# Performance work log

Hardware: AMD Instinct MI355X
Metric: run time of the kernel (lower is better)

Reference implementation:

```python
import jax, jax.numpy as jnp
import numpy as np

B, S, D, H = 4, 2048, 1024, 16
DH = D // H  # 64


def setup_inputs() -> dict:
    key = jax.random.key(0)
    ks = jax.random.split(key, 9)
    scale = 1.0 / np.sqrt(D)
    x = jax.random.normal(ks[0], (B, S, D), dtype=jnp.float32)
    # Stacked per-head projection weights, equivalent to ModuleList of Linear(D, DH)
    Wq = jax.random.uniform(ks[1], (H, D, DH), jnp.float32, -scale, scale)
    bq = jax.random.uniform(ks[2], (H, DH), jnp.float32, -scale, scale)
    Wk = jax.random.uniform(ks[3], (H, D, DH), jnp.float32, -scale, scale)
    bk = jax.random.uniform(ks[4], (H, DH), jnp.float32, -scale, scale)
    Wv = jax.random.uniform(ks[5], (H, D, DH), jnp.float32, -scale, scale)
    bv = jax.random.uniform(ks[6], (H, DH), jnp.float32, -scale, scale)
    Wo = jax.random.uniform(ks[7], (D, D), jnp.float32, -scale, scale)
    bo = jax.random.uniform(ks[8], (D,), jnp.float32, -scale, scale)
    return {"x": x, "Wq": Wq, "bq": bq, "Wk": Wk, "bk": bk,
            "Wv": Wv, "bv": bv, "Wo": Wo, "bo": bo}


def reference(x, Wq, bq, Wk, bk, Wv, bv, Wo, bo):
    # Per-head Linear projections, batched across heads: [B,S,D]x[H,D,DH] -> [B,H,S,DH]
    q = jnp.einsum('bsd,hde->bhse', x, Wq) + bq[None, :, None, :]
    k = jnp.einsum('bsd,hde->bhse', x, Wk) + bk[None, :, None, :]
    v = jnp.einsum('bsd,hde->bhse', x, Wv) + bv[None, :, None, :]
    # Scaled dot-product attention (no mask is applied in the original forward)
    scores = jnp.einsum('bhse,bhte->bhst', q, k) / jnp.sqrt(jnp.float32(DH))
    attn = jax.nn.softmax(scores, axis=-1)
    z = jnp.einsum('bhst,bhte->bhse', attn, v)  # [B,H,S,DH]
    # Concat heads on last dim (head-major order matches torch.cat over dim=-1)
    multihead = jnp.transpose(z, (0, 2, 1, 3)).reshape(B, S, D)
    return multihead @ Wo + bo
```

## Files before the change

### kernel.cpp

```cpp
#include <hip/hip_runtime.h>
#include <hip/hip_bf16.h>
#include <cstdint>
#include <cstddef>


typedef unsigned short u16;
typedef unsigned int u32;
typedef __attribute__((ext_vector_type(8))) __bf16 bf16x8;
typedef __attribute__((ext_vector_type(8))) unsigned short u16x8;
typedef __attribute__((ext_vector_type(4))) float f32x4;
typedef __attribute__((ext_vector_type(4))) unsigned int u32x4;

__device__ __forceinline__ u16 f2bf(float f) {
  union { __hip_bfloat16 h; u16 u; } c;
  c.h = __float2bfloat16(f);
  return c.u;
}
#if defined(__has_builtin)
#if __has_builtin(__builtin_amdgcn_cvt_pk_bf16_f32)
#define HAS_PK_BF16 1
#endif
#endif
__device__ __forceinline__ u32 pk2c(float a, float b) {
#ifdef HAS_PK_BF16
  return __builtin_bit_cast(u32, __builtin_amdgcn_cvt_pk_bf16_f32(a, b));
#else
  const u32 ua = __float_as_uint(a);
  const u32 ub = __float_as_uint(b);
  const u32 ra = ua + 0x7FFFu + ((ua >> 16) & 1u);
  const u32 rb = ub + 0x7FFFu + ((ub >> 16) & 1u);
  return (ra >> 16) | (rb & 0xFFFF0000u);
#endif
}
__device__ __forceinline__ float ex2(float x) {
  return __builtin_amdgcn_exp2f(x);
}

__device__ __forceinline__ void async16(const void* g, void* l) {
  __builtin_amdgcn_global_load_lds(
      (const __attribute__((address_space(1))) void*)g,
      (__attribute__((address_space(3))) void*)l, 16, 0, 0);
}

__global__ void k_pack_all(const float* __restrict__ x,
                           const float* __restrict__ Wq, const float* __restrict__ Wk,
                           const float* __restrict__ Wv,
                           const float* __restrict__ bq, const float* __restrict__ bk,
                           const float* __restrict__ bv,
                           const float* __restrict__ Wo,
                           u16* __restrict__ xb, u16* __restrict__ Wt,
                           float* __restrict__ bqkv, u16* __restrict__ Wot) {
  __shared__ __align__(16) u16 tile[64][72];
  const int bid = blockIdx.x;
  const int t = threadIdx.x;
  if (bid < 1024) {
    const float* src;
    u16* dstp;
    int rstride, n_base, d0;
    if (bid < 768) {
      const int proj = bid >> 8, h = (bid >> 4) & 15, dt = bid & 15;
      const float* Wp = (proj == 0) ? Wq : ((proj == 1) ? Wk : Wv);
      src = Wp + h * 65536 + (dt * 64) * 64;
      rstride = 64;
      n_base = proj * 1024 + h * 64;
      d0 = dt * 64;
      dstp = Wt;
    } else {
      const int tb = bid - 768, nt = tb >> 4, dt = tb & 15;
      src = Wo + (size_t)(dt * 64) * 1024 + nt * 64;
      rstride = 1024;
      n_base = nt * 64;
      d0 = dt * 64;
      dstp = Wot;
    }
    {
      const int row = t >> 2, c0 = (t & 3) * 16;
      const float* s = src + row * rstride + c0;
#pragma unroll
      for (int j = 0; j < 4; ++j) {
        const float4 v = *(const float4*)(s + j * 4);
        ushort4 o;
        o.x = f2bf(v.x); o.y = f2bf(v.y); o.z = f2bf(v.z); o.w = f2bf(v.w);
        *(ushort4*)&tile[row][c0 + j * 4] = o;
      }
    }
    __syncthreads();
    {
      const int e = t >> 2, c0 = (t & 3) * 16;
      u16 buf[16];
#pragma unroll
      for (int i = 0; i < 16; ++i) buf[i] = tile[c0 + i][e];
      u16* d = dstp + (size_t)(n_base + e) * 1024 + d0 + c0;
      *(u16x8*)d = *(const u16x8*)&buf[0];
      *(u16x8*)(d + 8) = *(const u16x8*)&buf[8];
    }
  } else if (bid < 9216) {
    const int i = ((bid - 1024) * 256 + t) * 4;
    const float4 v = *(const float4*)(x + i);
    ushort4 o;
    o.x = f2bf(v.x); o.y = f2bf(v.y); o.z = f2bf(v.z); o.w = f2bf(v.w);
    *(ushort4*)(xb + i) = o;
  } else {
    const int n = (bid - 9216) * 256 + t;
    const int proj = n >> 10, rem = n & 1023, h = rem >> 6, e = rem & 63;
    const float* bp = (proj == 0) ? bq : ((proj == 1) ? bk : bv);
    bqkv[n] = bp[h * 64 + e];
  }
}

template <int MODE>
__global__ __launch_bounds__(256)
void k_gemm(const u16* __restrict__ A, const u16* __restrict__ Bt,
            const float* __restrict__ bias, void* __restrict__ Cout, int ldc) {
  __shared__ __align__(16) u16 Alds[128 * 32];
  __shared__ __align__(16) u16 Blds[128 * 32];
  const int t = threadIdx.x;
  const int lane = t & 63;
  const int w = t >> 6;
  const int l15 = lane & 15;
  const int quad = lane >> 4;
  const int wm = w >> 1, wn = w & 1;
  const int m0 = blockIdx.y << 7;
  const int n0 = blockIdx.x << 7;

  const u16* ga0 = A + (size_t)(m0 + (t >> 2)) * 1024 + (t & 3) * 8;
  const u16* ga1 = ga0 + (size_t)64 * 1024;
  const u16* gb0 = Bt + (size_t)(n0 + (t >> 2)) * 1024 + (t & 3) * 8;
  const u16* gb1 = gb0 + (size_t)64 * 1024;
  u16* const lA0 = Alds + w * 512;
  u16* const lA1 = Alds + w * 512 + 2048;
  u16* const lB0 = Blds + w * 512;
  u16* const lB1 = Blds + w * 512 + 2048;

  f32x4 acc[4][4];
#pragma unroll
  for (int mi = 0; mi < 4; ++mi)
#pragma unroll
    for (int ni = 0; ni < 4; ++ni) acc[mi][ni] = (f32x4){0.f, 0.f, 0.f, 0.f};

  for (int k0 = 0; k0 < 1024; k0 += 32) {
    __syncthreads();
    async16(ga0, lA0); async16(ga1, lA1);
    async16(gb0, lB0); async16(gb1, lB1);
    ga0 += 32; ga1 += 32; gb0 += 32; gb1 += 32;
    __syncthreads();
    bf16x8 af[4], bfr[4];
#pragma unroll
    for (int i = 0; i < 4; ++i) {
      af[i]  = *(const bf16x8*)(Alds + (wm * 64 + i * 16 + l15) * 32 + quad * 8);
      bfr[i] = *(const bf16x8*)(Blds + (wn * 64 + i * 16 + l15) * 32 + quad * 8);
    }
#pragma unroll
    for (int mi = 0; mi < 4; ++mi)
#pragma unroll
      for (int ni = 0; ni < 4; ++ni)
        acc[mi][ni] = __builtin_amdgcn_mfma_f32_16x16x32_bf16(af[mi], bfr[ni], acc[mi][ni], 0, 0, 0);
  }

  const int row0 = m0 + wm * 64;
  const int col0 = n0 + wn * 64;
  const float qscale = (MODE == 0 && col0 < 1024) ? 0.125f * 1.4426950408889634f : 1.0f;
#pragma unroll
  for (int mi = 0; mi < 4; ++mi) {
#pragma unroll
    for (int ni = 0; ni < 4; ++ni) {
      const int col = col0 + ni * 16 + l15;
      const float bb = bias[col];
#pragma unroll
      for (int r = 0; r < 4; ++r) {
        const int row = row0 + mi * 16 + quad * 4 + r;
        const float v = (acc[mi][ni][r] + bb) * qscale;
        if (MODE == 0) ((u16*)Cout)[(size_t)row * ldc + col] = f2bf(v);
        else           ((float*)Cout)[(size_t)row * ldc + col] = v;
      }
    }
  }
}

__global__ __launch_bounds__(256)
void k_vt(const u16* __restrict__ qkv, u16* __restrict__ vtg) {
  __shared__ u16 tile[64][72];
  const int t = threadIdx.x;
  const int bh = blockIdx.y, b = bh >> 4, h = bh & 15;
  const int s0 = blockIdx.x << 6;
  {
    const int row = t >> 2, col0 = (t & 3) * 16;
    const u16* src = qkv + (size_t)(b * 2048 + s0 + row) * 3072 + 2048 + h * 64 + col0;
    const u16x8 v0 = *(const u16x8*)src;
    const u16x8 v1 = *(const u16x8*)(src + 8);
    *(u16x8*)&tile[row][col0] = v0;
    *(u16x8*)&tile[row][col0 + 8] = v1;
  }
  __syncthreads();
  {
    const int e = t >> 2, sc = (t & 3) * 16;
    u16 buf[16];
#pragma unroll
    for (int i = 0; i < 16; ++i) buf[i] = tile[sc + i][e];
    u16* dst = vtg + ((size_t)bh * 64 + e) * 2048 + s0 + sc;
    *(u16x8*)dst = *(const u16x8*)&buf[0];
    *(u16x8*)(dst + 8) = *(const u16x8*)&buf[8];
  }
}

__global__ __launch_bounds__(256)
void k_attn(const u16* __restrict__ qkv, const u16* __restrict__ vtg,
            u16* __restrict__ mh) {
  __shared__ __align__(16) u16 smem[16384];

  const int t = threadIdx.x;
  const int lane = t & 63;
  const int w = t >> 6;
  const int l15 = lane & 15;
  const int quad = lane >> 4;
  const int bh = blockIdx.x, b = bh >> 4, h = bh & 15;
  const int s0 = blockIdx.y << 7;

  const int lam0 = t >> 3;
  const int key0 = (lam0 & 3) | (((lam0 >> 2) & 3) << 3) | (((lam0 >> 4) & 1) << 2);
  const int ck = (t & 7) ^ (lam0 & 7);
  const u16* kbase = qkv + (size_t)(b * 2048 + key0) * 3072 + 1024 + h * 64 + ck * 8;
  const int e0 = t >> 3;
  const int cv = (t & 7) ^ (e0 & 7);
  const u16* vbase = vtg + ((size_t)bh * 64 + e0) * 2048 + cv * 8;

  const int kofs = w * 512;
  const int vofs = 4096 + w * 512;

  bf16x8 aq[2][2];
#pragma unroll
  for (int g = 0; g < 2; ++g)
#pragma unroll
    for (int ks2 = 0; ks2 < 2; ++ks2)
      aq[g][ks2] = *(const bf16x8*)(qkv +
          (size_t)(b * 2048 + s0 + w * 32 + g * 16 + l15) * 3072 +
          h * 64 + ks2 * 32 + quad * 8);

  const u32x4 onesu = (u32x4){0x3F803F80u, 0x3F803F80u, 0x3F803F80u, 0x3F803F80u};
  const bf16x8 ones = __builtin_bit_cast(bf16x8, onesu);

  f32x4 o[2][4];
  f32x4 lacc[2];
#pragma unroll
  for (int g = 0; g < 2; ++g) {
    lacc[g] = (f32x4){0.f, 0.f, 0.f, 0.f};
#pragma unroll
    for (int ne = 0; ne < 4; ++ne) o[g][ne] = (f32x4){0.f, 0.f, 0.f, 0.f};
  }

#pragma unroll
  for (int r = 0; r < 2; ++r) {
    async16(kbase + (size_t)r * (32 * 3072), smem + kofs + r * 2048);
    async16(vbase + (size_t)r * (32 * 2048), smem + vofs + r * 2048);
  }
  kbase += 64 * 3072;
  vbase += 64;

#pragma unroll 2
  for (int kt = 0; kt < 32; ++kt) {
    const int cur = kt & 1;
    const u16* const Kc = smem + cur * 8192;
    const u16* const Vc = Kc + 4096;
    u16* const nb = smem + (cur ^ 1) * 8192;

    __builtin_amdgcn_s_barrier();
#pragma unroll
    for (int r = 0; r < 2; ++r) {
      async16(kbase + (size_t)r * (32 * 3072), nb + kofs + r * 2048);
      async16(vbase + (size_t)r * (32 * 2048), nb + vofs + r * 2048);
    }
    kbase += 64 * 3072;
    vbase += 64;
    asm volatile("s_waitcnt vmcnt(4)" ::: "memory");
    __builtin_amdgcn_s_barrier();
    __builtin_amdgcn_sched_barrier(0);

#pragma unroll
    for (int ks = 0; ks < 2; ++ks) {
      u32x4 pf[2];
#pragma unroll
      for (int h2 = 0; h2 < 2; ++h2) {
        const int row = (ks * 2 + h2) * 16 + l15;
        const bf16x8 kf0 = *(const bf16x8*)(Kc + row * 64 + ((quad) ^ (l15 & 7)) * 8);
        const bf16x8 kf1 = *(const bf16x8*)(Kc + row * 64 + ((4 + quad) ^ (l15 & 7)) * 8);
        f32x4 st[2];
        __builtin_amdgcn_s_setprio(1);
#pragma unroll
        for (int g = 0; g < 2; ++g) {
          st[g] = __builtin_amdgcn_mfma_f32_16x16x32_bf16(kf0, aq[g][0], (f32x4){0.f,0.f,0.f,0.f}, 0, 0, 0);
          st[g] = __builtin_amdgcn_mfma_f32_16x16x32_bf16(kf1, aq[g][1], st[g], 0, 0, 0);
        }
        __builtin_amdgcn_s_setprio(0);
#pragma unroll
        for (int g = 0; g < 2; ++g) {
          const float p0 = ex2(st[g][0]), p1 = ex2(st[g][1]);
          const float p2 = ex2(st[g][2]), p3 = ex2(st[g][3]);
          pf[g][h2 * 2 + 0] = pk2c(p0, p1);
          pf[g][h2 * 2 + 1] = pk2c(p2, p3);
        }
      }
      __builtin_amdgcn_s_setprio(1);
#pragma unroll
      for (int ne = 0; ne < 4; ++ne) {
        const int e = ne * 16 + l15;
        const bf16x8 bv8 = *(const bf16x8*)(Vc + e * 64 + ((ks * 4 + quad) ^ (e & 7)) * 8);
#pragma unroll
        for (int g = 0; g < 2; ++g)
          o[g][ne] = __builtin_amdgcn_mfma_f32_16x16x32_bf16(
              __builtin_bit_cast(bf16x8, pf[g]), bv8, o[g][ne], 0, 0, 0);
      }
#pragma unroll
      for (int g = 0; g < 2; ++g)
        lacc[g] = __builtin_amdgcn_mfma_f32_16x16x32_bf16(
            __builtin_bit_cast(bf16x8, pf[g]), ones, lacc[g], 0, 0, 0);
      __builtin_amdgcn_s_setprio(0);
    }
  }

#pragma unroll
  for (int g = 0; g < 2; ++g) {
#pragma unroll
    for (int r = 0; r < 4; ++r) {
      const float iv = 1.f / lacc[g][r];
      const int row = s0 + w * 32 + g * 16 + quad * 4 + r;
#pragma unroll
      for (int ne = 0; ne < 4; ++ne) {
        const int col = h * 64 + ne * 16 + l15;
        mh[(size_t)(b * 2048 + row) * 1024 + col] = f2bf(o[g][ne][r] * iv);
      }
    }
  }
}

extern "C" void kernel_launch(void* const* d_in, const int* in_sizes, int n_in,
                              void* d_out, int out_size, void* d_ws, size_t ws_size,
                              hipStream_t stream) {
  (void)in_sizes; (void)n_in; (void)out_size; (void)ws_size;
  const float* x  = (const float*)d_in[0];
  const float* Wq = (const float*)d_in[1];
  const float* bq = (const float*)d_in[2];
  const float* Wk = (const float*)d_in[3];
  const float* bk = (const float*)d_in[4];
  const float* Wv = (const float*)d_in[5];
  const float* bv = (const float*)d_in[6];
  const float* Wo = (const float*)d_in[7];
  const float* bo = (const float*)d_in[8];

  char* ws = (char*)d_ws;
  u16*   Xb   = (u16*)  (ws + 0);
  u16*   Vtg  = (u16*)  (ws + 0);
  u16*   Wt   = (u16*)  (ws + 16777216);
  float* bqkv = (float*)(ws + 23068672);
  u16*   Wot  = (u16*)  (ws + 23080960);
  u16*   QKV  = (u16*)  (ws + 25178112);
  u16*   MH   = (u16*)  (ws + 75509760);
  float* out  = (float*)d_out;

  k_pack_all <<<9228, 256, 0, stream>>>(x, Wq, Wk, Wv, bq, bk, bv, Wo,
                                        Xb, Wt, bqkv, Wot);
  k_gemm<0>  <<<dim3(24, 64), 256, 0, stream>>>(Xb, Wt, bqkv, (void*)QKV, 3072);
  k_vt       <<<dim3(32, 64), 256, 0, stream>>>(QKV, Vtg);
  k_attn     <<<dim3(64, 16), 256, 0, stream>>>(QKV, Vtg, MH);
  k_gemm<1>  <<<dim3(8, 64), 256, 0, stream>>>(MH, Wot, bo, (void*)out, 1024);
}
```

Measured before the change: 296.7 us.

## Halve attention KV tile to 32 keys and hoist all LDS fragment loads

The attention kernel now streams 32 keys per iteration instead of 64, which halves LDS use (16 KB instead of 32 KB) and doubles the loop trip count. The V tile gets a new XOR swizzle for its 32-wide rows. All K and V fragment reads from LDS are issued at the top of each iteration, before the QK MFMAs, exp and PV MFMAs are grouped into separate phases. Lower LDS use may let more blocks reside per CU, but it adds barriers per key and gives less work between each prefetch and its wait.

```diff
diff --git a/kernel.cpp b/kernel.cpp
--- a/kernel.cpp
+++ b/kernel.cpp
@@ -206,7 +206,7 @@
 __global__ __launch_bounds__(256)
 void k_attn(const u16* __restrict__ qkv, const u16* __restrict__ vtg,
             u16* __restrict__ mh) {
-  __shared__ __align__(16) u16 smem[16384];
+  __shared__ __align__(16) u16 smem[8192];
 
   const int t = threadIdx.x;
   const int lane = t & 63;
@@ -220,12 +220,14 @@
   const int key0 = (lam0 & 3) | (((lam0 >> 2) & 3) << 3) | (((lam0 >> 4) & 1) << 2);
   const int ck = (t & 7) ^ (lam0 & 7);
   const u16* kbase = qkv + (size_t)(b * 2048 + key0) * 3072 + 1024 + h * 64 + ck * 8;
-  const int e0 = t >> 3;
-  const int cv = (t & 7) ^ (e0 & 7);
-  const u16* vbase = vtg + ((size_t)bh * 64 + e0) * 2048 + cv * 8;
+  const int ev = t >> 2;
+  const int cv = (t & 3) ^ (ev & 3) ^ ((ev >> 2) & 3);
+  const u16* vbase = vtg + ((size_t)bh * 64 + ev) * 2048 + cv * 8;
 
   const int kofs = w * 512;
-  const int vofs = 4096 + w * 512;
+  const int vofs = 2048 + w * 512;
+
+  const int fe = (l15 & 3) ^ (l15 >> 2);
 
   bf16x8 aq[2][2];
 #pragma unroll
@@ -248,73 +250,74 @@
     for (int ne = 0; ne < 4; ++ne) o[g][ne] = (f32x4){0.f, 0.f, 0.f, 0.f};
   }
 
-#pragma unroll
-  for (int r = 0; r < 2; ++r) {
-    async16(kbase + (size_t)r * (32 * 3072), smem + kofs + r * 2048);
-    async16(vbase + (size_t)r * (32 * 2048), smem + vofs + r * 2048);
-  }
-  kbase += 64 * 3072;
-  vbase += 64;
+  async16(kbase, smem + kofs);
+  async16(vbase, smem + vofs);
+  kbase += 32 * 3072;
+  vbase += 32;
 
 #pragma unroll 2
-  for (int kt = 0; kt < 32; ++kt) {
+  for (int kt = 0; kt < 64; ++kt) {
     const int cur = kt & 1;
-    const u16* const Kc = smem + cur * 8192;
-    const u16* const Vc = Kc + 4096;
-    u16* const nb = smem + (cur ^ 1) * 8192;
+    const u16* const Kc = smem + cur * 4096;
+    const u16* const Vc = Kc + 2048;
+    u16* const nb = smem + (cur ^ 1) * 4096;
 
     __builtin_amdgcn_s_barrier();
-#pragma unroll
-    for (int r = 0; r < 2; ++r) {
-      async16(kbase + (size_t)r * (32 * 3072), nb + kofs + r * 2048);
-      async16(vbase + (size_t)r * (32 * 2048), nb + vofs + r * 2048);
-    }
-    kbase += 64 * 3072;
-    vbase += 64;
-    asm volatile("s_waitcnt vmcnt(4)" ::: "memory");
+    async16(kbase, nb + kofs);
+    async16(vbase, nb + vofs);
+    kbase += 32 * 3072;
+    vbase += 32;
+    asm volatile("s_waitcnt vmcnt(2)" ::: "memory");
     __builtin_amdgcn_s_barrier();
     __builtin_amdgcn_sched_barrier(0);
 
-#pragma unroll
-    for (int ks = 0; ks < 2; ++ks) {
-      u32x4 pf[2];
+    bf16x8 kf[2][2], bvf[4];
+#pragma unroll
+    for (int h2 = 0; h2 < 2; ++h2) {
+      const int row = h2 * 16 + l15;
+      kf[h2][0] = *(const bf16x8*)(Kc + row * 64 + ((quad) ^ (l15 & 7)) * 8);
+      kf[h2][1] = *(const bf16x8*)(Kc + row * 64 + ((4 + quad) ^ (l15 & 7)) * 8);
+    }
+#pragma unroll
+    for (int ne = 0; ne < 4; ++ne) {
+      const int e = ne * 16 + l15;
+      bvf[ne] = *(const bf16x8*)(Vc + e * 32 + (quad ^ fe) * 8);
+    }
+
+    f32x4 st[2][2];
+    __builtin_amdgcn_s_setprio(1);
+#pragma unroll
+    for (int h2 = 0; h2 < 2; ++h2)
+#pragma unroll
+      for (int g = 0; g < 2; ++g) {
+        st[h2][g] = __builtin_amdgcn_mfma_f32_16x16x32_bf16(kf[h2][0], aq[g][0], (f32x4){0.f,0.f,0.f,0.f}, 0, 0, 0);
+        st[h2][g] = __builtin_amdgcn_mfma_f32_16x16x32_bf16(kf[h2][1], aq[g][1], st[h2][g], 0, 0, 0);
+      }
+    __builtin_amdgcn_s_setprio(0);
+
+    u32x4 pf[2];
+#pragma unroll
+    for (int g = 0; g < 2; ++g)
 #pragma unroll
       for (int h2 = 0; h2 < 2; ++h2) {
-        const int row = (ks * 2 + h2) * 16 + l15;
-        const bf16x8 kf0 = *(const bf16x8*)(Kc + row * 64 + ((quad) ^ (l15 & 7)) * 8);
-        const bf16x8 kf1 = *(const bf16x8*)(Kc + row * 64 + ((4 + quad) ^ (l15 & 7)) * 8);
-        f32x4 st[2];
-        __builtin_amdgcn_s_setprio(1);
-#pragma unroll
-        for (int g = 0; g < 2; ++g) {
-          st[g] = __builtin_amdgcn_mfma_f32_16x16x32_bf16(kf0, aq[g][0], (f32x4){0.f,0.f,0.f,0.f}, 0, 0, 0);
-          st[g] = __builtin_amdgcn_mfma_f32_16x16x32_bf16(kf1, aq[g][1], st[g], 0, 0, 0);
-        }
-        __builtin_amdgcn_s_setprio(0);
-#pragma unroll
-        for (int g = 0; g < 2; ++g) {
-          const float p0 = ex2(st[g][0]), p1 = ex2(st[g][1]);
-          const float p2 = ex2(st[g][2]), p3 = ex2(st[g][3]);
-          pf[g][h2 * 2 + 0] = pk2c(p0, p1);
-          pf[g][h2 * 2 + 1] = pk2c(p2, p3);
-        }
-      }
-      __builtin_amdgcn_s_setprio(1);
-#pragma unroll
-      for (int ne = 0; ne < 4; ++ne) {
-        const int e = ne * 16 + l15;
-        const bf16x8 bv8 = *(const bf16x8*)(Vc + e * 64 + ((ks * 4 + quad) ^ (e & 7)) * 8);
-#pragma unroll
-        for (int g = 0; g < 2; ++g)
-          o[g][ne] = __builtin_amdgcn_mfma_f32_16x16x32_bf16(
-              __builtin_bit_cast(bf16x8, pf[g]), bv8, o[g][ne], 0, 0, 0);
-      }
+        const float p0 = ex2(st[h2][g][0]), p1 = ex2(st[h2][g][1]);
+        const float p2 = ex2(st[h2][g][2]), p3 = ex2(st[h2][g][3]);
+        pf[g][h2 * 2 + 0] = pk2c(p0, p1);
+        pf[g][h2 * 2 + 1] = pk2c(p2, p3);
+      }
+
+    __builtin_amdgcn_s_setprio(1);
+#pragma unroll
+    for (int ne = 0; ne < 4; ++ne)
 #pragma unroll
       for (int g = 0; g < 2; ++g)
-        lacc[g] = __builtin_amdgcn_mfma_f32_16x16x32_bf16(
-            __builtin_bit_cast(bf16x8, pf[g]), ones, lacc[g], 0, 0, 0);
-      __builtin_amdgcn_s_setprio(0);
-    }
+        o[g][ne] = __builtin_amdgcn_mfma_f32_16x16x32_bf16(
+            __builtin_bit_cast(bf16x8, pf[g]), bvf[ne], o[g][ne], 0, 0, 0);
+#pragma unroll
+    for (int g = 0; g < 2; ++g)
+      lacc[g] = __builtin_amdgcn_mfma_f32_16x16x32_bf16(
+          __builtin_bit_cast(bf16x8, pf[g]), ones, lacc[g], 0, 0, 0);
+    __builtin_amdgcn_s_setprio(0);
   }
 
 #pragma unroll
```

Result: no change. 296.8 us (+0.0%).
